# Kernel optimization log

Hardware: AMD Instinct MI355X
Metric: run time of the kernel (lower is better)

Reference implementation:

```python
import jax, jax.numpy as jnp
import numpy as np

D = 1024
N_HEADS = 16
D_HEAD = D // N_HEADS


def setup_inputs() -> dict:
    key = jax.random.key(0)
    ks = jax.random.split(key, 7)
    B, S = 4, 1024
    x = jax.random.normal(ks[0], (B, S, D), dtype=jnp.float32)
    # per-head linear params, stacked over heads: W[h] is [d_head, d_head] (torch Linear weight),
    # y = s @ W[h].T + b[h]
    scale = 1.0 / np.sqrt(D_HEAD)
    Wq = jax.random.uniform(ks[1], (N_HEADS, D_HEAD, D_HEAD), jnp.float32, -scale, scale)
    Wk = jax.random.uniform(ks[2], (N_HEADS, D_HEAD, D_HEAD), jnp.float32, -scale, scale)
    Wv = jax.random.uniform(ks[3], (N_HEADS, D_HEAD, D_HEAD), jnp.float32, -scale, scale)
    bq = jax.random.uniform(ks[4], (N_HEADS, D_HEAD), jnp.float32, -scale, scale)
    bk = jax.random.uniform(ks[5], (N_HEADS, D_HEAD), jnp.float32, -scale, scale)
    bv = jax.random.uniform(ks[6], (N_HEADS, D_HEAD), jnp.float32, -scale, scale)
    return {"pix_sequences": x, "Wq": Wq, "Wk": Wk, "Wv": Wv,
            "bq": bq, "bk": bk, "bv": bv}


def reference(pix_sequences, Wq, Wk, Wv, bq, bk, bv):
    B, S, d = pix_sequences.shape
    # split feature dim into heads: [B, S, H, dh]
    xh = pix_sequences.reshape(B, S, N_HEADS, D_HEAD)
    # per-head linear: y = s @ W.T + b
    q = jnp.einsum('bshd,hed->bshe', xh, Wq) + bq  # [B,S,H,dh]
    k = jnp.einsum('bshd,hed->bshe', xh, Wk) + bk
    v = jnp.einsum('bshd,hed->bshe', xh, Wv) + bv
    scores = jnp.einsum('bqhd,bkhd->bhqk', q, k) / jnp.sqrt(jnp.float32(D_HEAD))
    attn = jax.nn.softmax(scores, axis=-1)  # [B,H,S,S]
    out = jnp.einsum('bhqk,bkhd->bqhd', attn, v)  # [B,S,H,dh]
    return out.reshape(B, S, d)
```

## Files before the change

### kernel.cpp

```cpp
#include <hip/hip_runtime.h>
#include <hip/hip_bf16.h>

constexpr int BB = 4;
constexpr int SS = 1024;
constexpr int HH = 16;
constexpr int DH = 64;
constexpr int DM = 1024;

using f32x16 = __attribute__((ext_vector_type(16))) float;
using s16x8  = __attribute__((ext_vector_type(8))) short;

__device__ __forceinline__ f32x16 mfma32(s16x8 a, s16x8 b, f32x16 c) {
    return __builtin_amdgcn_mfma_f32_32x32x16_bf16(a, b, c, 0, 0, 0);
}

__device__ __forceinline__ unsigned short bf16bits(float x) {
    union { __hip_bfloat16 h; unsigned short s; } cv;
    cv.h = __float2bfloat16(x);
    return cv.s;
}
__device__ __forceinline__ unsigned pk_bf16(float lo, float hi) {
    return (unsigned)bf16bits(lo) | ((unsigned)bf16bits(hi) << 16);
}

__device__ __forceinline__ float fast_exp2(float x) {
#if __has_builtin(__builtin_amdgcn_exp2f)
    return __builtin_amdgcn_exp2f(x);
#else
    return __expf(x * 0.6931471805599453f);
#endif
}

__global__ __launch_bounds__(256) void qkv_proj_kernel(
    const float* __restrict__ x,
    const float* __restrict__ Wq, const float* __restrict__ Wk, const float* __restrict__ Wv,
    const float* __restrict__ bq, const float* __restrict__ bk, const float* __restrict__ bv,
    __hip_bfloat16* __restrict__ q_ws, __hip_bfloat16* __restrict__ k_ws,
    __hip_bfloat16* __restrict__ v_ws)
{
    const int bid  = blockIdx.x;
    const int tile = bid & 7;
    const int pair = bid >> 3;
    const int b = pair >> 4, h = pair & 15;
    const int t = threadIdx.x;
    const int w = t >> 6, l = t & 63;
    const int lq = l & 31, hi = l >> 5;
    const int s0 = tile * 128;

    __shared__ __align__(16) char Xs[16384];
    __shared__ __align__(16) char Vt[16384];

    {
        const float* xb = x + (size_t)(b * SS + s0) * DM + h * DH;
        #pragma unroll
        for (int i = 0; i < 8; ++i) {
            const int c  = t + 256 * i;
            const int r  = c >> 4, cw = c & 15;
            float4 v4 = *reinterpret_cast<const float4*>(xb + (size_t)r * DM + cw * 4);
            uint2 p;
            p.x = pk_bf16(v4.x, v4.y);
            p.y = pk_bf16(v4.z, v4.w);
            *reinterpret_cast<uint2*>(Xs + r * 128 + ((cw * 8) ^ ((r & 7) << 4))) = p;
        }
    }
    __syncthreads();

    const int arow = w * 32 + lq;
    const int asw  = (arow & 7) << 4;
    s16x8 af[4];
    #pragma unroll
    for (int s = 0; s < 4; ++s)
        af[s] = *reinterpret_cast<const s16x8*>(Xs + arow * 128 + ((s * 32 + hi * 16) ^ asw));

    #pragma unroll
    for (int m = 0; m < 3; ++m) {
        const float* Wm = (m == 0) ? Wq : (m == 1) ? Wk : Wv;
        const float* bm = (m == 0) ? bq : (m == 1) ? bk : bv;

        f32x16 a0, a1;
        #pragma unroll
        for (int r = 0; r < 16; ++r) { a0[r] = 0.0f; a1[r] = 0.0f; }

        #pragma unroll
        for (int s = 0; s < 4; ++s) {
            const float* wp0 = Wm + (size_t)(h * DH + lq) * DH + s * 16 + hi * 8;
            const float* wp1 = wp0 + 32 * DH;
            float4 wa0 = reinterpret_cast<const float4*>(wp0)[0];
            float4 wb0 = reinterpret_cast<const float4*>(wp0)[1];
            float4 wa1 = reinterpret_cast<const float4*>(wp1)[0];
            float4 wb1 = reinterpret_cast<const float4*>(wp1)[1];
            union { unsigned u[4]; s16x8 v; } bf0, bf1;
            bf0.u[0] = pk_bf16(wa0.x, wa0.y); bf0.u[1] = pk_bf16(wa0.z, wa0.w);
            bf0.u[2] = pk_bf16(wb0.x, wb0.y); bf0.u[3] = pk_bf16(wb0.z, wb0.w);
            bf1.u[0] = pk_bf16(wa1.x, wa1.y); bf1.u[1] = pk_bf16(wa1.z, wa1.w);
            bf1.u[2] = pk_bf16(wb1.x, wb1.y); bf1.u[3] = pk_bf16(wb1.z, wb1.w);
            a0 = mfma32(af[s], bf0.v, a0);
            a1 = mfma32(af[s], bf1.v, a1);
        }

        const float bias0 = bm[h * DH + lq];
        const float bias1 = bm[h * DH + 32 + lq];

        if (m < 2) {
            __hip_bfloat16* dst = (m == 0) ? q_ws : k_ws;
            #pragma unroll
            for (int r = 0; r < 16; ++r) {
                const int qr = (r & 3) + 8 * (r >> 2) + 4 * hi;
                __hip_bfloat16* op = dst + ((size_t)pair * SS + s0 + w * 32 + qr) * DH;
                op[lq]      = __float2bfloat16(a0[r] + bias0);
                op[32 + lq] = __float2bfloat16(a1[r] + bias1);
            }
        } else {
            #pragma unroll
            for (int g = 0; g < 4; ++g) {
                const int off = w * 64 + g * 16 + hi * 8;
                uint2 p0, p1;
                p0.x = pk_bf16(a0[4*g+0] + bias0, a0[4*g+1] + bias0);
                p0.y = pk_bf16(a0[4*g+2] + bias0, a0[4*g+3] + bias0);
                p1.x = pk_bf16(a1[4*g+0] + bias1, a1[4*g+1] + bias1);
                p1.y = pk_bf16(a1[4*g+2] + bias1, a1[4*g+3] + bias1);
                *reinterpret_cast<uint2*>(Vt + lq * 256 + (off ^ ((lq & 7) << 4))) = p0;
                *reinterpret_cast<uint2*>(Vt + (32 + lq) * 256 + (off ^ (((32 + lq) & 7) << 4))) = p1;
            }
        }
    }
    __syncthreads();

    #pragma unroll
    for (int i = 0; i < 4; ++i) {
        const int c   = t + 256 * i;
        const int row = c >> 4, cc = c & 15;
        s16x8 val = *reinterpret_cast<const s16x8*>(
            Vt + row * 256 + ((cc * 16) ^ ((row & 7) << 4)));
        *reinterpret_cast<s16x8*>(v_ws + ((size_t)pair * DH + row) * SS + s0 + cc * 8) = val;
    }
}

__global__ __launch_bounds__(256) void attn_kernel(
    const __hip_bfloat16* __restrict__ q_ws,
    const __hip_bfloat16* __restrict__ k_ws,
    const __hip_bfloat16* __restrict__ v_ws,
    float* __restrict__ out)
{
    const int bid  = blockIdx.x;
    const int lbid = (bid & 7) * 64 + (bid >> 3);
    const int qt   = lbid & 7;
    const int pair = lbid >> 3;
    const int b = pair >> 4, h = pair & 15;
    const int t = threadIdx.x;
    const int w = t >> 6, l = t & 63;
    const int lq = l & 31, hi = l >> 5;

    __shared__ __align__(16) char Kl[8192];
    __shared__ __align__(16) char Vl[8192];

    const __hip_bfloat16* qp = q_ws + ((size_t)pair * SS + qt * 128 + w * 32 + lq) * DH + hi * 8;
    s16x8 qf[4];
    #pragma unroll
    for (int s5 = 0; s5 < 4; ++s5)
        qf[s5] = *reinterpret_cast<const s16x8*>(qp + s5 * 16);

    const int u0 = t, u1 = t + 256;
    const __hip_bfloat16* kb = k_ws + (size_t)pair * SS * DH;
    const __hip_bfloat16* vb = v_ws + (size_t)pair * DH * SS;
    const int ksw0 = (u0 ^ ((u0 >> 3) & 7)) * 16;
    const int ksw1 = (u1 ^ ((u1 >> 3) & 7)) * 16;
    const size_t voff0 = (size_t)(u0 >> 3) * SS + (u0 & 7) * 8;
    const size_t voff1 = (size_t)(u1 >> 3) * SS + (u1 & 7) * 8;

    s16x8 kr0 = *reinterpret_cast<const s16x8*>(kb + u0 * 8);
    s16x8 kr1 = *reinterpret_cast<const s16x8*>(kb + u1 * 8);
    s16x8 vr0 = *reinterpret_cast<const s16x8*>(vb + voff0);
    s16x8 vr1 = *reinterpret_cast<const s16x8*>(vb + voff1);

    f32x16 o0, o1;
    #pragma unroll
    for (int r = 0; r < 16; ++r) { o0[r] = 0.0f; o1[r] = 0.0f; }
    float m_run = -3.0e38f, lsum = 0.0f;
    const float cml = 0.18033688011112042f;

    const int kbase0 = lq * 128;
    const int kbase1 = (32 + lq) * 128;
    const int swz = (lq & 7) << 4;

    for (int kt = 0; kt < 16; ++kt) {
        __syncthreads();
        *reinterpret_cast<s16x8*>(Kl + ksw0) = kr0;
        *reinterpret_cast<s16x8*>(Kl + ksw1) = kr1;
        *reinterpret_cast<s16x8*>(Vl + ksw0) = vr0;
        *reinterpret_cast<s16x8*>(Vl + ksw1) = vr1;
        __syncthreads();
        if (kt < 15) {
            kr0 = *reinterpret_cast<const s16x8*>(kb + (kt + 1) * 4096 + u0 * 8);
            kr1 = *reinterpret_cast<const s16x8*>(kb + (kt + 1) * 4096 + u1 * 8);
            vr0 = *reinterpret_cast<const s16x8*>(vb + voff0 + (kt + 1) * 64);
            vr1 = *reinterpret_cast<const s16x8*>(vb + voff1 + (kt + 1) * 64);
        }

        f32x16 sc0, sc1;
        #pragma unroll
        for (int r = 0; r < 16; ++r) { sc0[r] = 0.0f; sc1[r] = 0.0f; }
        #pragma unroll
        for (int s5 = 0; s5 < 4; ++s5) {
            const int co = (2 * s5 + hi) << 4;
            s16x8 ka = *reinterpret_cast<const s16x8*>(Kl + kbase0 + (co ^ swz));
            sc0 = mfma32(ka, qf[s5], sc0);
        }
        #pragma unroll
        for (int s5 = 0; s5 < 4; ++s5) {
            const int co = (2 * s5 + hi) << 4;
            s16x8 ka = *reinterpret_cast<const s16x8*>(Kl + kbase1 + (co ^ swz));
            sc1 = mfma32(ka, qf[s5], sc1);
        }

        float mx = fmaxf(sc0[0], sc1[0]);
        #pragma unroll
        for (int r = 1; r < 16; ++r) mx = fmaxf(mx, fmaxf(sc0[r], sc1[r]));
        mx = fmaxf(mx, __shfl_xor(mx, 32));
        if (!__all((mx - m_run) * cml <= 8.0f)) {
            float mnew  = fmaxf(m_run, mx);
            float alpha = fast_exp2((m_run - mnew) * cml);
            lsum *= alpha;
            #pragma unroll
            for (int r = 0; r < 16; ++r) { o0[r] *= alpha; o1[r] *= alpha; }
            m_run = mnew;
        }
        const float nm = -m_run * cml;
        float rs = 0.0f;
        #pragma unroll
        for (int r = 0; r < 16; ++r) {
            sc0[r] = fast_exp2(fmaf(sc0[r], cml, nm));
            sc1[r] = fast_exp2(fmaf(sc1[r], cml, nm));
            rs += sc0[r] + sc1[r];
        }
        rs += __shfl_xor(rs, 32);
        lsum += rs;

        #pragma unroll
        for (int s5 = 0; s5 < 4; ++s5) {
            const int sb8 = (s5 & 1) * 8;
            unsigned a0, b0, a1, b1;
            if (s5 < 2) {
                a0 = pk_bf16(sc0[sb8 + 0], sc0[sb8 + 1]);
                b0 = pk_bf16(sc0[sb8 + 4], sc0[sb8 + 5]);
                a1 = pk_bf16(sc0[sb8 + 2], sc0[sb8 + 3]);
                b1 = pk_bf16(sc0[sb8 + 6], sc0[sb8 + 7]);
            } else {
                a0 = pk_bf16(sc1[sb8 + 0], sc1[sb8 + 1]);
                b0 = pk_bf16(sc1[sb8 + 4], sc1[sb8 + 5]);
                a1 = pk_bf16(sc1[sb8 + 2], sc1[sb8 + 3]);
                b1 = pk_bf16(sc1[sb8 + 6], sc1[sb8 + 7]);
            }
            const unsigned sa0 = (unsigned)__shfl_xor((int)a0, 32);
            const unsigned sb0 = (unsigned)__shfl_xor((int)b0, 32);
            const unsigned sa1 = (unsigned)__shfl_xor((int)a1, 32);
            const unsigned sb1 = (unsigned)__shfl_xor((int)b1, 32);
            union { unsigned u[4]; s16x8 v; } afr;
            afr.u[0] = hi ? sb0 : a0;
            afr.u[1] = hi ? sb1 : a1;
            afr.u[2] = hi ? b0 : sa0;
            afr.u[3] = hi ? b1 : sa1;
            const int co = (2 * s5 + hi) << 4;
            s16x8 vb0 = *reinterpret_cast<const s16x8*>(Vl + kbase0 + (co ^ swz));
            o0 = mfma32(afr.v, vb0, o0);
            s16x8 vb1 = *reinterpret_cast<const s16x8*>(Vl + kbase1 + (co ^ swz));
            o1 = mfma32(afr.v, vb1, o1);
        }
    }

    const float inv = 1.0f / lsum;
    #pragma unroll
    for (int r = 0; r < 16; ++r) {
        const int qr = (r & 3) + 8 * (r >> 2) + 4 * hi;
        const float invr = __shfl(inv, qr);
        float* op = out + ((size_t)b * SS + qt * 128 + w * 32 + qr) * DM + h * DH + lq;
        op[0]  = o0[r] * invr;
        op[32] = o1[r] * invr;
    }
}

extern "C" void kernel_launch(void* const* d_in, const int* in_sizes, int n_in,
                              void* d_out, int out_size, void* d_ws, size_t ws_size,
                              hipStream_t stream) {
    const float* x  = (const float*)d_in[0];
    const float* Wq = (const float*)d_in[1];
    const float* Wk = (const float*)d_in[2];
    const float* Wv = (const float*)d_in[3];
    const float* bq = (const float*)d_in[4];
    const float* bk = (const float*)d_in[5];
    const float* bv = (const float*)d_in[6];
    float* out = (float*)d_out;

    __hip_bfloat16* q_ws = (__hip_bfloat16*)d_ws;
    __hip_bfloat16* k_ws = q_ws + (size_t)BB * HH * SS * DH;
    __hip_bfloat16* v_ws = k_ws + (size_t)BB * HH * SS * DH;

    qkv_proj_kernel<<<dim3(BB * HH * (SS / 128)), dim3(256), 0, stream>>>(
        x, Wq, Wk, Wv, bq, bk, bv, q_ws, k_ws, v_ws);
    attn_kernel<<<dim3(BB * HH * (SS / 64 / 2)), dim3(256), 0, stream>>>(
        q_ws, k_ws, v_ws, out);
}
```

Before: 59.62 us.

## Double-buffer K/V tiles in attention and stage Q/K stores through LDS

The attention kernel now keeps two LDS buffers for K and V. Each tile's LDS write moves to the end of the previous iteration, so the loop needs one barrier per tile instead of two. The projection kernel writes Q and K through swizzled LDS and then issues coalesced 16-byte global stores instead of scattered 2-byte stores. The row max and row sum reductions become tree reductions to shorten dependency chains. The cost is more LDS per block, which may lower occupancy.

```diff
diff --git a/kernel.cpp b/kernel.cpp
--- a/kernel.cpp
+++ b/kernel.cpp
@@ -48,6 +48,7 @@
     const int s0 = tile * 128;
 
     __shared__ __align__(16) char Xs[16384];
+    __shared__ __align__(16) char Kt[16384];
     __shared__ __align__(16) char Vt[16384];
 
     {
@@ -71,6 +72,7 @@
     #pragma unroll
     for (int s = 0; s < 4; ++s)
         af[s] = *reinterpret_cast<const s16x8*>(Xs + arow * 128 + ((s * 32 + hi * 16) ^ asw));
+    __syncthreads();
 
     #pragma unroll
     for (int m = 0; m < 3; ++m) {
@@ -102,13 +104,15 @@
         const float bias1 = bm[h * DH + 32 + lq];
 
         if (m < 2) {
-            __hip_bfloat16* dst = (m == 0) ? q_ws : k_ws;
+            char* T = (m == 0) ? Xs : Kt;
             #pragma unroll
             for (int r = 0; r < 16; ++r) {
-                const int qr = (r & 3) + 8 * (r >> 2) + 4 * hi;
-                __hip_bfloat16* op = dst + ((size_t)pair * SS + s0 + w * 32 + qr) * DH;
-                op[lq]      = __float2bfloat16(a0[r] + bias0);
-                op[32 + lq] = __float2bfloat16(a1[r] + bias1);
+                const int row = w * 32 + (r & 3) + 8 * (r >> 2) + 4 * hi;
+                const int sw  = (row & 7) << 4;
+                *reinterpret_cast<unsigned short*>(T + row * 128 + ((lq * 2) ^ sw)) =
+                    bf16bits(a0[r] + bias0);
+                *reinterpret_cast<unsigned short*>(T + row * 128 + (((32 + lq) * 2) ^ sw)) =
+                    bf16bits(a1[r] + bias1);
             }
         } else {
             #pragma unroll
@@ -129,10 +133,20 @@
     #pragma unroll
     for (int i = 0; i < 4; ++i) {
         const int c   = t + 256 * i;
+        const int row = c >> 3, cc = c & 7;
+        const int off = row * 128 + ((cc * 16) ^ ((row & 7) << 4));
+        s16x8 qv = *reinterpret_cast<const s16x8*>(Xs + off);
+        *reinterpret_cast<s16x8*>(q_ws + ((size_t)pair * SS + s0 + row) * DH + cc * 8) = qv;
+        s16x8 kv = *reinterpret_cast<const s16x8*>(Kt + off);
+        *reinterpret_cast<s16x8*>(k_ws + ((size_t)pair * SS + s0 + row) * DH + cc * 8) = kv;
+    }
+    #pragma unroll
+    for (int i = 0; i < 4; ++i) {
+        const int c   = t + 256 * i;
         const int row = c >> 4, cc = c & 15;
-        s16x8 val = *reinterpret_cast<const s16x8*>(
+        s16x8 vv = *reinterpret_cast<const s16x8*>(
             Vt + row * 256 + ((cc * 16) ^ ((row & 7) << 4)));
-        *reinterpret_cast<s16x8*>(v_ws + ((size_t)pair * DH + row) * SS + s0 + cc * 8) = val;
+        *reinterpret_cast<s16x8*>(v_ws + ((size_t)pair * DH + row) * SS + s0 + cc * 8) = vv;
     }
 }
 
@@ -151,8 +165,8 @@
     const int w = t >> 6, l = t & 63;
     const int lq = l & 31, hi = l >> 5;
 
-    __shared__ __align__(16) char Kl[8192];
-    __shared__ __align__(16) char Vl[8192];
+    __shared__ __align__(16) char Kl[2][8192];
+    __shared__ __align__(16) char Vl[2][8192];
 
     const __hip_bfloat16* qp = q_ws + ((size_t)pair * SS + qt * 128 + w * 32 + lq) * DH + hi * 8;
     s16x8 qf[4];
@@ -168,10 +182,17 @@
     const size_t voff0 = (size_t)(u0 >> 3) * SS + (u0 & 7) * 8;
     const size_t voff1 = (size_t)(u1 >> 3) * SS + (u1 & 7) * 8;
 
-    s16x8 kr0 = *reinterpret_cast<const s16x8*>(kb + u0 * 8);
-    s16x8 kr1 = *reinterpret_cast<const s16x8*>(kb + u1 * 8);
-    s16x8 vr0 = *reinterpret_cast<const s16x8*>(vb + voff0);
-    s16x8 vr1 = *reinterpret_cast<const s16x8*>(vb + voff1);
+    {
+        s16x8 k0 = *reinterpret_cast<const s16x8*>(kb + u0 * 8);
+        s16x8 k1 = *reinterpret_cast<const s16x8*>(kb + u1 * 8);
+        s16x8 v0 = *reinterpret_cast<const s16x8*>(vb + voff0);
+        s16x8 v1 = *reinterpret_cast<const s16x8*>(vb + voff1);
+        *reinterpret_cast<s16x8*>(Kl[0] + ksw0) = k0;
+        *reinterpret_cast<s16x8*>(Kl[0] + ksw1) = k1;
+        *reinterpret_cast<s16x8*>(Vl[0] + ksw0) = v0;
+        *reinterpret_cast<s16x8*>(Vl[0] + ksw1) = v1;
+    }
+    __syncthreads();
 
     f32x16 o0, o1;
     #pragma unroll
@@ -183,19 +204,17 @@
     const int kbase1 = (32 + lq) * 128;
     const int swz = (lq & 7) << 4;
 
+    int p = 0;
+    s16x8 kr0, kr1, vr0, vr1;
     for (int kt = 0; kt < 16; ++kt) {
-        __syncthreads();
-        *reinterpret_cast<s16x8*>(Kl + ksw0) = kr0;
-        *reinterpret_cast<s16x8*>(Kl + ksw1) = kr1;
-        *reinterpret_cast<s16x8*>(Vl + ksw0) = vr0;
-        *reinterpret_cast<s16x8*>(Vl + ksw1) = vr1;
-        __syncthreads();
         if (kt < 15) {
             kr0 = *reinterpret_cast<const s16x8*>(kb + (kt + 1) * 4096 + u0 * 8);
             kr1 = *reinterpret_cast<const s16x8*>(kb + (kt + 1) * 4096 + u1 * 8);
             vr0 = *reinterpret_cast<const s16x8*>(vb + voff0 + (kt + 1) * 64);
             vr1 = *reinterpret_cast<const s16x8*>(vb + voff1 + (kt + 1) * 64);
         }
+        const char* Kp = Kl[p];
+        const char* Vp = Vl[p];
 
         f32x16 sc0, sc1;
         #pragma unroll
@@ -203,20 +222,26 @@
         #pragma unroll
         for (int s5 = 0; s5 < 4; ++s5) {
             const int co = (2 * s5 + hi) << 4;
-            s16x8 ka = *reinterpret_cast<const s16x8*>(Kl + kbase0 + (co ^ swz));
+            s16x8 ka = *reinterpret_cast<const s16x8*>(Kp + kbase0 + (co ^ swz));
             sc0 = mfma32(ka, qf[s5], sc0);
         }
         #pragma unroll
         for (int s5 = 0; s5 < 4; ++s5) {
             const int co = (2 * s5 + hi) << 4;
-            s16x8 ka = *reinterpret_cast<const s16x8*>(Kl + kbase1 + (co ^ swz));
+            s16x8 ka = *reinterpret_cast<const s16x8*>(Kp + kbase1 + (co ^ swz));
             sc1 = mfma32(ka, qf[s5], sc1);
         }
 
-        float mx = fmaxf(sc0[0], sc1[0]);
-        #pragma unroll
-        for (int r = 1; r < 16; ++r) mx = fmaxf(mx, fmaxf(sc0[r], sc1[r]));
-        mx = fmaxf(mx, __shfl_xor(mx, 32));
+        float tm[16];
+        #pragma unroll
+        for (int r = 0; r < 16; ++r) tm[r] = fmaxf(sc0[r], sc1[r]);
+        #pragma unroll
+        for (int s = 8; s >= 1; s >>= 1)
+            #pragma unroll
+            for (int r = 0; r < 8; ++r)
+                if (r < s) tm[r] = fmaxf(tm[r], tm[r + s]);
+        float mx = fmaxf(tm[0], __shfl_xor(tm[0], 32));
+
         if (!__all((mx - m_run) * cml <= 8.0f)) {
             float mnew  = fmaxf(m_run, mx);
             float alpha = fast_exp2((m_run - mnew) * cml);
@@ -226,15 +251,19 @@
             m_run = mnew;
         }
         const float nm = -m_run * cml;
-        float rs = 0.0f;
+        float ts[16];
         #pragma unroll
         for (int r = 0; r < 16; ++r) {
             sc0[r] = fast_exp2(fmaf(sc0[r], cml, nm));
             sc1[r] = fast_exp2(fmaf(sc1[r], cml, nm));
-            rs += sc0[r] + sc1[r];
-        }
-        rs += __shfl_xor(rs, 32);
-        lsum += rs;
+            ts[r]  = sc0[r] + sc1[r];
+        }
+        #pragma unroll
+        for (int s = 8; s >= 1; s >>= 1)
+            #pragma unroll
+            for (int r = 0; r < 8; ++r)
+                if (r < s) ts[r] += ts[r + s];
+        lsum += ts[0] + __shfl_xor(ts[0], 32);
 
         #pragma unroll
         for (int s5 = 0; s5 < 4; ++s5) {
@@ -261,11 +290,20 @@
             afr.u[2] = hi ? b0 : sa0;
             afr.u[3] = hi ? b1 : sa1;
             const int co = (2 * s5 + hi) << 4;
-            s16x8 vb0 = *reinterpret_cast<const s16x8*>(Vl + kbase0 + (co ^ swz));
+            s16x8 vb0 = *reinterpret_cast<const s16x8*>(Vp + kbase0 + (co ^ swz));
             o0 = mfma32(afr.v, vb0, o0);
-            s16x8 vb1 = *reinterpret_cast<const s16x8*>(Vl + kbase1 + (co ^ swz));
+            s16x8 vb1 = *reinterpret_cast<const s16x8*>(Vp + kbase1 + (co ^ swz));
             o1 = mfma32(afr.v, vb1, o1);
         }
+
+        if (kt < 15) {
+            *reinterpret_cast<s16x8*>(Kl[p ^ 1] + ksw0) = kr0;
+            *reinterpret_cast<s16x8*>(Kl[p ^ 1] + ksw1) = kr1;
+            *reinterpret_cast<s16x8*>(Vl[p ^ 1] + ksw0) = vr0;
+            *reinterpret_cast<s16x8*>(Vl[p ^ 1] + ksw1) = vr1;
+        }
+        __syncthreads();
+        p ^= 1;
     }
 
     const float inv = 1.0f / lsum;
```

Result: no change. 60.02 us (+0.7%).
